# Kernel tuning notes

Hardware: AMD Instinct MI355X
Metric: run time of the kernel (lower is better)

The kernel has to match this reference:

```python
import jax, jax.numpy as jnp
import numpy as np

HIDDEN = 1024
INTER = 4096
N_EXPERTS = 8
TOP_K = 2


def setup_inputs() -> dict:
    key = jax.random.key(0)
    ks = jax.random.split(key, 5)
    B, S = 2, 1024
    scale_h = 1.0 / np.sqrt(HIDDEN)
    scale_i = 1.0 / np.sqrt(INTER)
    return {
        "hidden_states": jax.random.normal(ks[0], (B, S, HIDDEN), dtype=jnp.float32),
        "router_w": jax.random.normal(ks[1], (N_EXPERTS, HIDDEN), dtype=jnp.float32) * scale_h,
        "gate_w": jax.random.normal(ks[2], (N_EXPERTS, INTER, HIDDEN), dtype=jnp.float32) * scale_h,
        "up_w": jax.random.normal(ks[3], (N_EXPERTS, INTER, HIDDEN), dtype=jnp.float32) * scale_h,
        "down_w": jax.random.normal(ks[4], (N_EXPERTS, HIDDEN, INTER), dtype=jnp.float32) * scale_i,
        "top_k": TOP_K,
    }


def reference(hidden_states, router_w, gate_w, up_w, down_w, top_k):
    B, S, D = hidden_states.shape
    E = router_w.shape[0]
    x = hidden_states.reshape(-1, D)              # [T, D]
    T = x.shape[0]

    router_logits = x @ router_w.T                # [T, E]
    probs = jax.nn.softmax(router_logits.astype(jnp.float32), axis=-1)
    routing_weights, selected = jax.lax.top_k(probs, top_k)   # [T, k]
    routing_weights = routing_weights.astype(x.dtype)

    # Dense combine weights: w[t, e] = routing weight if expert e selected for token t else 0
    combine = jnp.zeros((T, E), x.dtype).at[jnp.arange(T)[:, None], selected].add(routing_weights)

    # SwiGLU expert MLPs, computed for all experts then combined (same math as gather/scatter loop)
    g = jnp.einsum('td,ehd->eth', x, gate_w)      # [E, T, H]
    u = jnp.einsum('td,ehd->eth', x, up_w)        # [E, T, H]
    h = jax.nn.silu(g) * u
    expert_out = jnp.einsum('eth,edh->etd', h, down_w)  # [E, T, D]
    out = jnp.einsum('etd,te->td', expert_out, combine)  # [T, D]

    return out.reshape(B, S, D), router_logits
```

## Files before the change

kernel.cpp:

```cpp
#include <hip/hip_runtime.h>
#include <hip/hip_bf16.h>

#define HIDDEN 1024
#define INTER 4096
#define NEXP 8
#define T_TOK 2048

typedef short bf16x8 __attribute__((ext_vector_type(8)));
typedef float f32x4 __attribute__((ext_vector_type(4)));

#define CHUNK(row, kq) ((unsigned int)((row) * 64u + ((((unsigned int)(kq)) ^ ((((unsigned int)(row)) >> 1) & 3u)) << 4)))

__device__ __forceinline__ unsigned short f2bf(float f) {
    union { float f; unsigned int u; } v; v.f = f;
    return (unsigned short)(v.u >> 16);
}

__device__ __forceinline__ uint4 pack8trunc(float4 a, float4 b) {
    union { float4 f; unsigned short s[8]; } x, y; x.f = a; y.f = b;
    uint4 r;
    r.x = (unsigned int)x.s[1] | ((unsigned int)x.s[3] << 16);
    r.y = (unsigned int)x.s[5] | ((unsigned int)x.s[7] << 16);
    r.z = (unsigned int)y.s[1] | ((unsigned int)y.s[3] << 16);
    r.w = (unsigned int)y.s[5] | ((unsigned int)y.s[7] << 16);
    return r;
}

__device__ __forceinline__ void block_sync() {
    asm volatile("s_waitcnt lgkmcnt(0)" ::: "memory");
    __builtin_amdgcn_s_barrier();
    asm volatile("" ::: "memory");
}

__global__ void router_kernel(const float* __restrict__ x,
                              const float* __restrict__ rw,
                              float* __restrict__ logits_out,
                              int* __restrict__ counts,
                              int* __restrict__ ids,
                              float* __restrict__ wts,
                              int* __restrict__ tsel) {
    int t = blockIdx.x * 4 + (threadIdx.x >> 6);
    int lane = threadIdx.x & 63;
    if (t >= T_TOK) return;
    const float4* xr = (const float4*)(x + (size_t)t * HIDDEN);
    float acc[NEXP];
#pragma unroll
    for (int e = 0; e < NEXP; e++) acc[e] = 0.f;
#pragma unroll
    for (int c = 0; c < 4; c++) {
        float4 xv = xr[lane + c * 64];
#pragma unroll
        for (int e = 0; e < NEXP; e++) {
            float4 wv = ((const float4*)(rw + (size_t)e * HIDDEN))[lane + c * 64];
            acc[e] += xv.x * wv.x + xv.y * wv.y + xv.z * wv.z + xv.w * wv.w;
        }
    }
#pragma unroll
    for (int e = 0; e < NEXP; e++) {
        float v = acc[e];
        for (int off = 32; off >= 1; off >>= 1) v += __shfl_xor(v, off, 64);
        acc[e] = v;
    }
    if (lane == 0) {
        float* lo = logits_out + (size_t)t * NEXP;
        float mx = acc[0];
#pragma unroll
        for (int e = 1; e < NEXP; e++) mx = fmaxf(mx, acc[e]);
        float p[NEXP], s = 0.f;
#pragma unroll
        for (int e = 0; e < NEXP; e++) { p[e] = __expf(acc[e] - mx); s += p[e]; }
        float inv = 1.f / s;
#pragma unroll
        for (int e = 0; e < NEXP; e++) { p[e] *= inv; lo[e] = acc[e]; }
        int i1 = 0;
#pragma unroll
        for (int e = 1; e < NEXP; e++) if (p[e] > p[i1]) i1 = e;
        int i2 = (i1 == 0) ? 1 : 0;
#pragma unroll
        for (int e = 0; e < NEXP; e++) if (e != i1 && e != i2 && p[e] > p[i2]) i2 = e;
        int s1 = atomicAdd(&counts[i1], 1);
        ids[i1 * T_TOK + s1] = t; wts[i1 * T_TOK + s1] = p[i1];
        int s2 = atomicAdd(&counts[i2], 1);
        ids[i2 * T_TOK + s2] = t; wts[i2 * T_TOK + s2] = p[i2];
        tsel[t * 2]     = i1 * T_TOK + s1;
        tsel[t * 2 + 1] = i2 * T_TOK + s2;
    }
}

__global__ void scan_kernel(const int* __restrict__ counts, int* __restrict__ offsets) {
    if (threadIdx.x == 0) {
        int s = 0;
        for (int e = 0; e < NEXP; e++) { offsets[e] = s; s += counts[e]; }
    }
}

__global__ __launch_bounds__(1024) void gemm_gu(
    const float* __restrict__ x, const float* __restrict__ gw, const float* __restrict__ uw,
    const int* __restrict__ counts, const int* __restrict__ offsets,
    const int* __restrict__ ids, unsigned short* __restrict__ h) {
    const int e = blockIdx.z;
    const int cnt = counts[e];
    const int mt = blockIdx.y;
    if (mt * 256 >= cnt) return;
    const int nt = blockIdx.x;
    const int tid = threadIdx.x;
    const int lane = tid & 63, wid = tid >> 6;
    const int wm = wid >> 2, wn = wid & 3;

    __shared__ __align__(16) char bufE[32768];
    __shared__ __align__(16) char bufO[32768];

    const int arow = tid >> 2, akq = tid & 3;
    int ali = mt * 256 + arow; if (ali >= cnt) ali = cnt - 1;
    const unsigned int aoff = (unsigned int)(ids[e * T_TOK + ali] * HIDDEN + akq * 8);
    const unsigned int wAo = CHUNK(arow, akq);
    const int bsel = tid >> 9;
    const int bi = tid & 511;
    const int brow = bi >> 2, bkq = bi & 3;
    const float* bsrc = (bsel ? uw : gw) + (size_t)e * INTER * HIDDEN
                        + (size_t)(nt * 128 + brow) * HIDDEN + bkq * 8;
    const unsigned int wBo = 16384u + ((unsigned int)bsel << 13) + CHUNK(brow, bkq);

    f32x4 accg[4][2], accu[4][2];
#pragma unroll
    for (int mf = 0; mf < 4; mf++)
#pragma unroll
        for (int nf = 0; nf < 2; nf++)
#pragma unroll
            for (int v = 0; v < 4; v++) { accg[mf][nf][v] = 0.f; accu[mf][nf][v] = 0.f; }

    float4 s0, s1, t0, t1;
    s0 = *(const float4*)(x + aoff); s1 = *(const float4*)(x + aoff + 4);
    t0 = *(const float4*)(bsrc);     t1 = *(const float4*)(bsrc + 4);
    *(uint4*)(bufE + wAo) = pack8trunc(s0, s1);
    *(uint4*)(bufE + wBo) = pack8trunc(t0, t1);
    s0 = *(const float4*)(x + aoff + 32); s1 = *(const float4*)(x + aoff + 36);
    t0 = *(const float4*)(bsrc + 32);     t1 = *(const float4*)(bsrc + 36);
    block_sync();

    const unsigned int kqr = (unsigned int)(lane >> 4);
    const unsigned int rl = (unsigned int)(lane & 15);

#define GU_BODY(KT, RB, WB)                                                             \
    {                                                                                   \
        bf16x8 fa[4];                                                                   \
        _Pragma("unroll")                                                               \
        for (int mf = 0; mf < 4; mf++)                                                  \
            fa[mf] = *(const bf16x8*)((RB) + CHUNK(wm * 64 + mf * 16 + rl, kqr));       \
        if ((KT) + 1 < 32) {                                                            \
            *(uint4*)((WB) + wAo) = pack8trunc(s0, s1);                                 \
            *(uint4*)((WB) + wBo) = pack8trunc(t0, t1);                                 \
        }                                                                               \
        if ((KT) + 2 < 32) {                                                            \
            const int ko = ((KT) + 2) * 32;                                             \
            s0 = *(const float4*)(x + aoff + ko); s1 = *(const float4*)(x + aoff + ko + 4); \
            t0 = *(const float4*)(bsrc + ko);     t1 = *(const float4*)(bsrc + ko + 4); \
        }                                                                               \
        _Pragma("unroll")                                                               \
        for (int nf = 0; nf < 2; nf++) {                                                \
            const unsigned int br = wn * 32 + nf * 16 + rl;                             \
            bf16x8 bg = *(const bf16x8*)((RB) + 16384 + CHUNK(br, kqr));                \
            bf16x8 bu = *(const bf16x8*)((RB) + 24576 + CHUNK(br, kqr));                \
            _Pragma("unroll")                                                           \
            for (int mf = 0; mf < 4; mf++) {                                            \
                accg[mf][nf] = __builtin_amdgcn_mfma_f32_16x16x32_bf16(fa[mf], bg, accg[mf][nf], 0, 0, 0); \
                accu[mf][nf] = __builtin_amdgcn_mfma_f32_16x16x32_bf16(fa[mf], bu, accu[mf][nf], 0, 0, 0); \
            }                                                                           \
        }                                                                               \
        block_sync();                                                                   \
    }

    for (int kt = 0; kt < 32; kt += 2) {
        GU_BODY(kt, bufE, bufO)
        GU_BODY(kt + 1, bufO, bufE)
    }
#undef GU_BODY

    const int hoff = offsets[e];
#pragma unroll
    for (int mf = 0; mf < 4; mf++)
#pragma unroll
        for (int v = 0; v < 4; v++) {
            int il = wm * 64 + mf * 16 + ((lane >> 4) << 2) + v;
            int i = mt * 256 + il;
            if (i < cnt) {
                size_t rowbase = (size_t)(hoff + i) * INTER + nt * 128 + wn * 32 + (lane & 15);
#pragma unroll
                for (int nf = 0; nf < 2; nf++) {
                    float g = accg[mf][nf][v], u = accu[mf][nf][v];
                    float sg = g / (1.f + __expf(-g));
                    h[rowbase + nf * 16] = f2bf(sg * u);
                }
            }
        }
}

__global__ __launch_bounds__(512) void gemm_down(
    const unsigned short* __restrict__ h, const float* __restrict__ dw,
    const int* __restrict__ counts, const int* __restrict__ offsets,
    const float* __restrict__ wts, float* __restrict__ y) {
    const int ez = blockIdx.z;
    const int e = ez >> 1, ksp = ez & 1;
    const int cnt = counts[e];
    const int mt = blockIdx.y;
    if (mt * 128 >= cnt) return;
    const int nt = blockIdx.x;
    const int tid = threadIdx.x;
    const int lane = tid & 63, wid = tid >> 6;
    const int wm = wid >> 2, wn = wid & 3;

    __shared__ __align__(16) char bufE[16384];
    __shared__ __align__(16) char bufO[16384];

    const int hoff = offsets[e];
    const float* dbase = dw + (size_t)e * HIDDEN * INTER;

    const int row = tid >> 2, kq = tid & 3;
    int li = mt * 128 + row; if (li >= cnt) li = cnt - 1;
    const unsigned int aoff = (unsigned int)((hoff + li) * INTER + ksp * 2048 + kq * 8);
    const unsigned int wAo = CHUNK(row, kq);
    const unsigned int boff = (unsigned int)((nt * 128 + row) * INTER + ksp * 2048 + kq * 8);
    const unsigned int wBo = 8192u + CHUNK(row, kq);

    f32x4 acc[4][2];
#pragma unroll
    for (int mf = 0; mf < 4; mf++)
#pragma unroll
        for (int nf = 0; nf < 2; nf++)
#pragma unroll
            for (int v = 0; v < 4; v++) acc[mf][nf][v] = 0.f;

    int4 av; float4 b0, b1;
    av = *(const int4*)(h + aoff);
    b0 = *(const float4*)(dbase + boff); b1 = *(const float4*)(dbase + boff + 4);
    *(int4*)(bufE + wAo) = av;
    *(uint4*)(bufE + wBo) = pack8trunc(b0, b1);
    av = *(const int4*)(h + aoff + 32);
    b0 = *(const float4*)(dbase + boff + 32); b1 = *(const float4*)(dbase + boff + 36);
    block_sync();

    const unsigned int kqr = (unsigned int)(lane >> 4);
    const unsigned int rl = (unsigned int)(lane & 15);

#define DN_BODY(KT, RB, WB)                                                             \
    {                                                                                   \
        bf16x8 fa[4];                                                                   \
        _Pragma("unroll")                                                               \
        for (int mf = 0; mf < 4; mf++)                                                  \
            fa[mf] = *(const bf16x8*)((RB) + CHUNK(wm * 64 + mf * 16 + rl, kqr));       \
        if ((KT) + 1 < 64) {                                                            \
            *(int4*)((WB) + wAo) = av;                                                  \
            *(uint4*)((WB) + wBo) = pack8trunc(b0, b1);                                 \
        }                                                                               \
        if ((KT) + 2 < 64) {                                                            \
            const int ko = ((KT) + 2) * 32;                                             \
            av = *(const int4*)(h + aoff + ko);                                         \
            b0 = *(const float4*)(dbase + boff + ko); b1 = *(const float4*)(dbase + boff + ko + 4); \
        }                                                                               \
        _Pragma("unroll")                                                               \
        for (int nf = 0; nf < 2; nf++) {                                                \
            bf16x8 b = *(const bf16x8*)((RB) + 8192 + CHUNK(wn * 32 + nf * 16 + rl, kqr)); \
            _Pragma("unroll")                                                           \
            for (int mf = 0; mf < 4; mf++)                                              \
                acc[mf][nf] = __builtin_amdgcn_mfma_f32_16x16x32_bf16(fa[mf], b, acc[mf][nf], 0, 0, 0); \
        }                                                                               \
        block_sync();                                                                   \
    }

    for (int kt = 0; kt < 64; kt += 2) {
        DN_BODY(kt, bufE, bufO)
        DN_BODY(kt + 1, bufO, bufE)
    }
#undef DN_BODY

#pragma unroll
    for (int mf = 0; mf < 4; mf++)
#pragma unroll
        for (int v = 0; v < 4; v++) {
            int il = wm * 64 + mf * 16 + ((lane >> 4) << 2) + v;
            int i = mt * 128 + il;
            if (i < cnt) {
                float w = wts[e * T_TOK + i];
                float* yrow = y + ((size_t)ksp * 4096 + hoff + i) * HIDDEN
                                + nt * 128 + wn * 32 + (lane & 15);
#pragma unroll
                for (int nf = 0; nf < 2; nf++)
                    yrow[nf * 16] = w * acc[mf][nf][v];
            }
        }
}

__global__ __launch_bounds__(256) void combine_kernel(
    const float* __restrict__ y, const int* __restrict__ offsets,
    const int* __restrict__ tsel, float* __restrict__ out) {
    const int t = blockIdx.x;
    const int d = threadIdx.x * 4;
    int p0 = tsel[t * 2], p1 = tsel[t * 2 + 1];
    size_t g0 = (size_t)(offsets[p0 >> 11] + (p0 & (T_TOK - 1)));
    size_t g1 = (size_t)(offsets[p1 >> 11] + (p1 & (T_TOK - 1)));
    float4 a0 = *(const float4*)(y + g0 * HIDDEN + d);
    float4 a1 = *(const float4*)(y + (4096 + g0) * HIDDEN + d);
    float4 b0 = *(const float4*)(y + g1 * HIDDEN + d);
    float4 b1 = *(const float4*)(y + (4096 + g1) * HIDDEN + d);
    float4 o;
    o.x = (a0.x + a1.x) + (b0.x + b1.x);
    o.y = (a0.y + a1.y) + (b0.y + b1.y);
    o.z = (a0.z + a1.z) + (b0.z + b1.z);
    o.w = (a0.w + a1.w) + (b0.w + b1.w);
    *(float4*)(out + (size_t)t * HIDDEN + d) = o;
}

extern "C" void kernel_launch(void* const* d_in, const int* in_sizes, int n_in,
                              void* d_out, int out_size, void* d_ws, size_t ws_size,
                              hipStream_t stream) {
    const float* x  = (const float*)d_in[0];
    const float* rw = (const float*)d_in[1];
    const float* gw = (const float*)d_in[2];
    const float* uw = (const float*)d_in[3];
    const float* dw = (const float*)d_in[4];
    float* out = (float*)d_out;
    float* logits = out + (size_t)T_TOK * HIDDEN;

    char* ws = (char*)d_ws;
    int*   counts  = (int*)ws;
    int*   offsets = (int*)(ws + 32);
    int*   tsel    = (int*)(ws + 1024);
    int*   ids     = (int*)(ws + 20480);
    float* wts     = (float*)(ws + 90112);
    unsigned short* h = (unsigned short*)(ws + 262144);
    float* y       = (float*)(ws + 262144 + 33554432);

    hipMemsetAsync(counts, 0, 8 * sizeof(int), stream);

    router_kernel<<<T_TOK / 4, 256, 0, stream>>>(x, rw, logits, counts, ids, wts, tsel);
    scan_kernel<<<1, 64, 0, stream>>>(counts, offsets);
    gemm_gu<<<dim3(INTER / 128, 8, NEXP), 1024, 0, stream>>>(x, gw, uw, counts, offsets, ids, h);
    gemm_down<<<dim3(HIDDEN / 128, 16, NEXP * 2), 512, 0, stream>>>(h, dw, counts, offsets, wts, y);
    combine_kernel<<<T_TOK, 256, 0, stream>>>(y, offsets, tsel, out);
}
```

Measured before the change: 294.2 us.

## Use four LDS buffers to halve barriers and raise MFMA wave priority

Both expert GEMM kernels (gate/up and down) move from a two-buffer LDS ping-pong with a barrier after every K step to a four-buffer scheme. Two K steps run between block barriers, and the prologue preloads two stages instead of one. The MFMA section of each step is wrapped in s_setprio(1)/s_setprio(0) so the scheduler favours waves that are issuing matrix ops. The aim is to cut barrier stalls. In exchange, LDS use doubles: 128KB per block in gemm_gu and 64KB in gemm_down, which can lower occupancy.

```diff
diff --git a/kernel.cpp b/kernel.cpp
--- a/kernel.cpp
+++ b/kernel.cpp
@@ -107,8 +107,10 @@
     const int lane = tid & 63, wid = tid >> 6;
     const int wm = wid >> 2, wn = wid & 3;
 
-    __shared__ __align__(16) char bufE[32768];
-    __shared__ __align__(16) char bufO[32768];
+    __shared__ __align__(16) char lb0[32768];
+    __shared__ __align__(16) char lb1[32768];
+    __shared__ __align__(16) char lb2[32768];
+    __shared__ __align__(16) char lb3[32768];
 
     const int arow = tid >> 2, akq = tid & 3;
     int ali = mt * 256 + arow; if (ali >= cnt) ali = cnt - 1;
@@ -130,32 +132,37 @@
             for (int v = 0; v < 4; v++) { accg[mf][nf][v] = 0.f; accu[mf][nf][v] = 0.f; }
 
     float4 s0, s1, t0, t1;
-    s0 = *(const float4*)(x + aoff); s1 = *(const float4*)(x + aoff + 4);
-    t0 = *(const float4*)(bsrc);     t1 = *(const float4*)(bsrc + 4);
-    *(uint4*)(bufE + wAo) = pack8trunc(s0, s1);
-    *(uint4*)(bufE + wBo) = pack8trunc(t0, t1);
+    s0 = *(const float4*)(x + aoff);      s1 = *(const float4*)(x + aoff + 4);
+    t0 = *(const float4*)(bsrc);          t1 = *(const float4*)(bsrc + 4);
+    *(uint4*)(lb0 + wAo) = pack8trunc(s0, s1);
+    *(uint4*)(lb0 + wBo) = pack8trunc(t0, t1);
     s0 = *(const float4*)(x + aoff + 32); s1 = *(const float4*)(x + aoff + 36);
     t0 = *(const float4*)(bsrc + 32);     t1 = *(const float4*)(bsrc + 36);
+    *(uint4*)(lb1 + wAo) = pack8trunc(s0, s1);
+    *(uint4*)(lb1 + wBo) = pack8trunc(t0, t1);
+    s0 = *(const float4*)(x + aoff + 64); s1 = *(const float4*)(x + aoff + 68);
+    t0 = *(const float4*)(bsrc + 64);     t1 = *(const float4*)(bsrc + 68);
     block_sync();
 
     const unsigned int kqr = (unsigned int)(lane >> 4);
     const unsigned int rl = (unsigned int)(lane & 15);
 
-#define GU_BODY(KT, RB, WB)                                                             \
+#define GU_HALF(KT, RB, WB)                                                             \
     {                                                                                   \
         bf16x8 fa[4];                                                                   \
         _Pragma("unroll")                                                               \
         for (int mf = 0; mf < 4; mf++)                                                  \
             fa[mf] = *(const bf16x8*)((RB) + CHUNK(wm * 64 + mf * 16 + rl, kqr));       \
-        if ((KT) + 1 < 32) {                                                            \
+        if ((KT) + 2 < 32) {                                                            \
             *(uint4*)((WB) + wAo) = pack8trunc(s0, s1);                                 \
             *(uint4*)((WB) + wBo) = pack8trunc(t0, t1);                                 \
         }                                                                               \
-        if ((KT) + 2 < 32) {                                                            \
-            const int ko = ((KT) + 2) * 32;                                             \
+        if ((KT) + 3 < 32) {                                                            \
+            const int ko = ((KT) + 3) * 32;                                             \
             s0 = *(const float4*)(x + aoff + ko); s1 = *(const float4*)(x + aoff + ko + 4); \
             t0 = *(const float4*)(bsrc + ko);     t1 = *(const float4*)(bsrc + ko + 4); \
         }                                                                               \
+        __builtin_amdgcn_s_setprio(1);                                                  \
         _Pragma("unroll")                                                               \
         for (int nf = 0; nf < 2; nf++) {                                                \
             const unsigned int br = wn * 32 + nf * 16 + rl;                             \
@@ -167,14 +174,18 @@
                 accu[mf][nf] = __builtin_amdgcn_mfma_f32_16x16x32_bf16(fa[mf], bu, accu[mf][nf], 0, 0, 0); \
             }                                                                           \
         }                                                                               \
-        block_sync();                                                                   \
-    }
-
-    for (int kt = 0; kt < 32; kt += 2) {
-        GU_BODY(kt, bufE, bufO)
-        GU_BODY(kt + 1, bufO, bufE)
-    }
-#undef GU_BODY
+        __builtin_amdgcn_s_setprio(0);                                                  \
+    }
+
+    for (int kt = 0; kt < 32; kt += 4) {
+        GU_HALF(kt,     lb0, lb2)
+        GU_HALF(kt + 1, lb1, lb3)
+        block_sync();
+        GU_HALF(kt + 2, lb2, lb0)
+        GU_HALF(kt + 3, lb3, lb1)
+        block_sync();
+    }
+#undef GU_HALF
 
     const int hoff = offsets[e];
 #pragma unroll
@@ -209,8 +220,10 @@
     const int lane = tid & 63, wid = tid >> 6;
     const int wm = wid >> 2, wn = wid & 3;
 
-    __shared__ __align__(16) char bufE[16384];
-    __shared__ __align__(16) char bufO[16384];
+    __shared__ __align__(16) char lb0[16384];
+    __shared__ __align__(16) char lb1[16384];
+    __shared__ __align__(16) char lb2[16384];
+    __shared__ __align__(16) char lb3[16384];
 
     const int hoff = offsets[e];
     const float* dbase = dw + (size_t)e * HIDDEN * INTER;
@@ -232,31 +245,36 @@
 
     int4 av; float4 b0, b1;
     av = *(const int4*)(h + aoff);
-    b0 = *(const float4*)(dbase + boff); b1 = *(const float4*)(dbase + boff + 4);
-    *(int4*)(bufE + wAo) = av;
-    *(uint4*)(bufE + wBo) = pack8trunc(b0, b1);
+    b0 = *(const float4*)(dbase + boff);      b1 = *(const float4*)(dbase + boff + 4);
+    *(int4*)(lb0 + wAo) = av;
+    *(uint4*)(lb0 + wBo) = pack8trunc(b0, b1);
     av = *(const int4*)(h + aoff + 32);
     b0 = *(const float4*)(dbase + boff + 32); b1 = *(const float4*)(dbase + boff + 36);
+    *(int4*)(lb1 + wAo) = av;
+    *(uint4*)(lb1 + wBo) = pack8trunc(b0, b1);
+    av = *(const int4*)(h + aoff + 64);
+    b0 = *(const float4*)(dbase + boff + 64); b1 = *(const float4*)(dbase + boff + 68);
     block_sync();
 
     const unsigned int kqr = (unsigned int)(lane >> 4);
     const unsigned int rl = (unsigned int)(lane & 15);
 
-#define DN_BODY(KT, RB, WB)                                                             \
+#define DN_HALF(KT, RB, WB)                                                             \
     {                                                                                   \
         bf16x8 fa[4];                                                                   \
         _Pragma("unroll")                                                               \
         for (int mf = 0; mf < 4; mf++)                                                  \
             fa[mf] = *(const bf16x8*)((RB) + CHUNK(wm * 64 + mf * 16 + rl, kqr));       \
-        if ((KT) + 1 < 64) {                                                            \
+        if ((KT) + 2 < 64) {                                                            \
             *(int4*)((WB) + wAo) = av;                                                  \
             *(uint4*)((WB) + wBo) = pack8trunc(b0, b1);                                 \
         }                                                                               \
-        if ((KT) + 2 < 64) {                                                            \
-            const int ko = ((KT) + 2) * 32;                                             \
+        if ((KT) + 3 < 64) {                                                            \
+            const int ko = ((KT) + 3) * 32;                                             \
             av = *(const int4*)(h + aoff + ko);                                         \
             b0 = *(const float4*)(dbase + boff + ko); b1 = *(const float4*)(dbase + boff + ko + 4); \
         }                                                                               \
+        __builtin_amdgcn_s_setprio(1);                                                  \
         _Pragma("unroll")                                                               \
         for (int nf = 0; nf < 2; nf++) {                                                \
             bf16x8 b = *(const bf16x8*)((RB) + 8192 + CHUNK(wn * 32 + nf * 16 + rl, kqr)); \
@@ -264,14 +282,18 @@
             for (int mf = 0; mf < 4; mf++)                                              \
                 acc[mf][nf] = __builtin_amdgcn_mfma_f32_16x16x32_bf16(fa[mf], b, acc[mf][nf], 0, 0, 0); \
         }                                                                               \
-        block_sync();                                                                   \
-    }
-
-    for (int kt = 0; kt < 64; kt += 2) {
-        DN_BODY(kt, bufE, bufO)
-        DN_BODY(kt + 1, bufO, bufE)
-    }
-#undef DN_BODY
+        __builtin_amdgcn_s_setprio(0);                                                  \
+    }
+
+    for (int kt = 0; kt < 64; kt += 4) {
+        DN_HALF(kt,     lb0, lb2)
+        DN_HALF(kt + 1, lb1, lb3)
+        block_sync();
+        DN_HALF(kt + 2, lb2, lb0)
+        DN_HALF(kt + 3, lb3, lb1)
+        block_sync();
+    }
+#undef DN_HALF
 
 #pragma unroll
     for (int mf = 0; mf < 4; mf++)
```

Result: slower. 395.9 us (+34.6%).
